# Optimization experiments

Measured on AMD Instinct MI355X. Metric: run time of the kernel, lower is better.

Reference implementation:

```python
import jax, jax.numpy as jnp
import numpy as np

B, N, IN_F, H, DEG, L = 4096, 64, 32, 128, 8, 2
E = N * DEG
ALPHA = 0.2  # LeakyReLU slope
EPS = 1e-5   # LayerNorm eps


def setup_inputs() -> dict:
    key = jax.random.key(0)
    ks = jax.random.split(key, 16)
    # ring graph: node i -> (i+k) mod N for k=1..DEG (unique edges, every node has out-edges)
    src = jnp.repeat(jnp.arange(N, dtype=jnp.int32), DEG)
    dst = ((src + jnp.tile(jnp.arange(1, DEG + 1, dtype=jnp.int32), N)) % N).astype(jnp.int32)
    edge_index = jnp.stack([src, dst])  # (2, E)
    Hh = H // 2
    inp = {
        "x": jax.random.normal(ks[0], (B, IN_F), jnp.float32),
        "station_idx": jax.random.randint(ks[1], (B,), 0, N, jnp.int32),
        "edge_index": edge_index,
        "edge_weight": jax.random.uniform(ks[2], (E,), jnp.float32, 0.1, 1.0),
        "Wp": jax.random.normal(ks[3], (IN_F, H), jnp.float32) / np.sqrt(IN_F),
        "bp": jnp.zeros((H,), jnp.float32),
        "emb": jax.random.normal(ks[4], (N, Hh), jnp.float32) * 0.02,
        "gat_W": jax.random.normal(ks[5], (L, H, H), jnp.float32) / np.sqrt(H),
        "gat_a": jax.random.normal(ks[6], (L, 2 * H), jnp.float32) * 0.1,
        "W1": jax.random.normal(ks[7], (H + Hh, H), jnp.float32) / np.sqrt(H + Hh),
        "b1": jnp.zeros((H,), jnp.float32),
        "g1": jnp.ones((H,), jnp.float32),
        "be1": jnp.zeros((H,), jnp.float32),
        "W2": jax.random.normal(ks[8], (H, Hh), jnp.float32) / np.sqrt(H),
        "b2": jnp.zeros((Hh,), jnp.float32),
        "g2": jnp.ones((Hh,), jnp.float32),
        "be2": jnp.zeros((Hh,), jnp.float32),
        "Wo": jax.random.normal(ks[9], (Hh, 1), jnp.float32) / np.sqrt(Hh),
        "bo": jnp.zeros((1,), jnp.float32),
    }
    return inp


def _layernorm(v, g, b):
    m = v.mean(-1, keepdims=True)
    var = ((v - m) ** 2).mean(-1, keepdims=True)
    return (v - m) / jnp.sqrt(var + EPS) * g + b


def _gat(h, W, a, src, dst, edge_weight):
    # h: (B, N, H); W: (H, H); a: (2H,)
    Wh = jnp.einsum('bnf,fg->bng', h, W)
    s_src = Wh @ a[:H]   # (B, N)
    s_dst = Wh @ a[H:]   # (B, N)
    e = jax.nn.leaky_relu(s_src[:, src] + s_dst[:, dst], ALPHA)  # (B, E)
    e = e * edge_weight[None, :]
    att = jnp.zeros((h.shape[0], N, N), h.dtype).at[:, src, dst].set(e)
    mask = att == 0  # faithfully reproduces the torch zero-mask trick
    att = jnp.where(mask, -jnp.inf, att)
    att = jax.nn.softmax(att, axis=2)
    att = jnp.where(mask, 0.0, att)
    # dropout is identity at inference
    return jax.nn.elu(jnp.einsum('bnm,bmf->bnf', att, Wh))


def reference(x, station_idx, edge_index, edge_weight, Wp, bp, emb, gat_W, gat_a,
              W1, b1, g1, be1, W2, b2, g2, be2, Wo, bo):
    src, dst = edge_index[0], edge_index[1]
    h0 = x @ Wp + bp                               # (B, H)
    h = jnp.broadcast_to(h0[:, None, :], (x.shape[0], N, H))
    for i in range(L):
        h = h + _gat(h, gat_W[i], gat_a[i], src, dst, edge_weight)
    h_node = h[jnp.arange(x.shape[0]), station_idx]  # (B, H)
    s = emb[station_idx]                              # (B, H//2)
    z = jnp.concatenate([h_node, s], axis=-1)
    z = jax.nn.relu(_layernorm(z @ W1 + b1, g1, be1))
    z = jax.nn.relu(_layernorm(z @ W2 + b2, g2, be2))
    return (z @ Wo + bo).squeeze(-1)                  # (B,)
```

## Files before the change

kernel.cpp:

```cpp
#include <hip/hip_runtime.h>
#include <math.h>

namespace {

constexpr int SPW  = 8;
constexpr int ACTW = 196;
constexpr float LNEPS = 1e-5f;

typedef __attribute__((ext_vector_type(8))) __bf16 bf16x8;
typedef __attribute__((ext_vector_type(4))) float  f32x4;

template<int V> struct ic { static constexpr int value = V; };

template<int N, int I = 0, class F>
__device__ __forceinline__ void sfor(F&& f) {
    if constexpr (I < N) { f(ic<I>{}); sfor<N, I + 1>(f); }
}

__device__ __forceinline__ float elu1(float v) {
    return v > 0.f ? v : (__expf(v) - 1.f);
}

__global__ __launch_bounds__(64) void pack_weights(
    const float* __restrict__ Wp, const float* __restrict__ gatW,
    const float* __restrict__ W1, const float* __restrict__ W2,
    __bf16* __restrict__ wsf)
{
    const int f = blockIdx.x;
    const int l = threadIdx.x;
    const float* src; int kt, nt, N;
    if (f < 8)        { src = Wp;            kt = 0;            nt = f;            N = 128; }
    else if (f < 40)  { int r = f - 8;  src = gatW;         kt = r >> 3; nt = r & 7; N = 128; }
    else if (f < 72)  { int r = f - 40; src = gatW + 16384; kt = r >> 3; nt = r & 7; N = 128; }
    else if (f < 120) { int r = f - 72; src = W1;           kt = r / 8;  nt = r % 8; N = 128; }
    else              { int r = f - 120; src = W2;          kt = r >> 2; nt = r & 3; N = 64;  }
    const int k0 = kt * 32 + (l >> 4) * 8;
    const int n  = nt * 16 + (l & 15);
    bf16x8 v;
    sfor<8>([&](auto E) {
        v[E.value] = (__bf16)src[(size_t)(k0 + E.value) * N + n];
    });
    *reinterpret_cast<bf16x8*>(wsf + ((size_t)f * 64 + l) * 8) = v;
}

__global__ __launch_bounds__(64) void mfma_fused(
    const float* __restrict__ x, const int* __restrict__ sid,
    const __bf16* __restrict__ wsf,
    const float* __restrict__ bp, const float* __restrict__ emb,
    const float* __restrict__ b1, const float* __restrict__ g1,
    const float* __restrict__ be1,
    const float* __restrict__ b2, const float* __restrict__ g2,
    const float* __restrict__ be2,
    const float* __restrict__ Wo, const float* __restrict__ bo,
    float* __restrict__ out)
{
    __shared__ float act[16 * ACTW];

    const int l  = threadIdx.x;
    const int gq = l >> 4;
    const int j  = l & 15;
    const int sbase = blockIdx.x * SPW;

    {
        const int s = l >> 2, ch = l & 3;
        float4 v0 = {0.f, 0.f, 0.f, 0.f}, v1 = v0;
        if (s < SPW) {
            const float* xp = x + (size_t)(sbase + s) * 32 + ch * 8;
            v0 = *reinterpret_cast<const float4*>(xp);
            v1 = *reinterpret_cast<const float4*>(xp + 4);
        }
        float* dst = act + s * ACTW + ch * 8;
        *reinterpret_cast<float4*>(dst)     = v0;
        *reinterpret_cast<float4*>(dst + 4) = v1;
    }

    auto gemm = [&]<int NKT, int NNT>(ic<NKT>, ic<NNT>, int fbase, f32x4 (&acc)[NNT]) {
        const __bf16* fb = wsf + ((size_t)fbase * 64 + l) * 8;
        bf16x8 bq0[NNT], bq1[NNT];
        auto ldkt = [&](auto KT, bf16x8 (&bq)[NNT]) {
            sfor<NNT>([&](auto NT) {
                bq[NT.value] = *reinterpret_cast<const bf16x8*>(
                    fb + (size_t)(decltype(KT)::value * NNT + NT.value) * 512);
            });
        };
        auto akt = [&](auto KT) -> bf16x8 {
            const float* p = act + j * ACTW + decltype(KT)::value * 32 + gq * 8;
            const float4 f0 = *reinterpret_cast<const float4*>(p);
            const float4 f1 = *reinterpret_cast<const float4*>(p + 4);
            bf16x8 a;
            a[0] = (__bf16)f0.x; a[1] = (__bf16)f0.y; a[2] = (__bf16)f0.z; a[3] = (__bf16)f0.w;
            a[4] = (__bf16)f1.x; a[5] = (__bf16)f1.y; a[6] = (__bf16)f1.z; a[7] = (__bf16)f1.w;
            return a;
        };
        auto mm = [&](bf16x8 a, bf16x8 (&bq)[NNT]) {
            sfor<NNT>([&](auto NT) {
                acc[NT.value] = __builtin_amdgcn_mfma_f32_16x16x32_bf16(
                    a, bq[NT.value], acc[NT.value], 0, 0, 0);
            });
        };
        ldkt(ic<0>{}, bq0);
        sfor<NKT>([&](auto KT) {
            constexpr int kt = decltype(KT)::value;
            if constexpr (kt + 1 < NKT) {
                if constexpr (((kt + 1) & 1) == 0) ldkt(ic<kt + 1>{}, bq0);
                else                               ldkt(ic<kt + 1>{}, bq1);
            }
            const bf16x8 a = akt(KT);
            if constexpr ((kt & 1) == 0) mm(a, bq0); else mm(a, bq1);
        });
    };

    auto writeC = [&](f32x4 (&C)[8]) {
        sfor<8>([&](auto NT) { sfor<4>([&](auto R) {
            act[(4 * gq + R.value) * ACTW + NT.value * 16 + j] = C[NT.value][R.value];
        }); });
    };

    float bpv[8];
    sfor<8>([&](auto NT) { bpv[NT.value] = bp[NT.value * 16 + j]; });

    f32x4 hC[8];

    {
        f32x4 acc[8] = {};
        gemm(ic<1>{}, ic<8>{}, 0, acc);
        sfor<8>([&](auto NT) { sfor<4>([&](auto R) {
            hC[NT.value][R.value] = acc[NT.value][R.value] + bpv[NT.value];
        }); });
    }
    writeC(hC);

    {
        f32x4 acc[8] = {};
        gemm(ic<4>{}, ic<8>{}, 8, acc);
        sfor<8>([&](auto NT) { sfor<4>([&](auto R) {
            hC[NT.value][R.value] += elu1(acc[NT.value][R.value]);
        }); });
    }
    writeC(hC);

    {
        f32x4 acc[8] = {};
        gemm(ic<4>{}, ic<8>{}, 40, acc);
        sfor<8>([&](auto NT) { sfor<4>([&](auto R) {
            hC[NT.value][R.value] += elu1(acc[NT.value][R.value]);
        }); });
    }
    writeC(hC);

    {
        const int s = l >> 2, ch = l & 3;
        float4 e0 = {0.f,0.f,0.f,0.f}, e1 = e0, e2 = e0, e3 = e0;
        if (s < SPW) {
            const int st = sid[sbase + s];
            const float* ep = emb + (size_t)st * 64 + ch * 16;
            e0 = *reinterpret_cast<const float4*>(ep);
            e1 = *reinterpret_cast<const float4*>(ep + 4);
            e2 = *reinterpret_cast<const float4*>(ep + 8);
            e3 = *reinterpret_cast<const float4*>(ep + 12);
        }
        float* dst = act + s * ACTW + 128 + ch * 16;
        *reinterpret_cast<float4*>(dst)      = e0;
        *reinterpret_cast<float4*>(dst + 4)  = e1;
        *reinterpret_cast<float4*>(dst + 8)  = e2;
        *reinterpret_cast<float4*>(dst + 12) = e3;
    }

    {
        f32x4 acc[8] = {};
        gemm(ic<6>{}, ic<8>{}, 72, acc);
        float b1v[8], g1v[8], be1v[8];
        sfor<8>([&](auto NT) {
            b1v[NT.value]  = b1[NT.value * 16 + j];
            g1v[NT.value]  = g1[NT.value * 16 + j];
            be1v[NT.value] = be1[NT.value * 16 + j];
        });
        float su[4] = {}, sq[4] = {};
        sfor<8>([&](auto NT) { sfor<4>([&](auto R) {
            const float u = acc[NT.value][R.value] + b1v[NT.value];
            acc[NT.value][R.value] = u;
            su[R.value] += u; sq[R.value] += u * u;
        }); });
#pragma unroll
        for (int off = 1; off <= 8; off <<= 1) {
            sfor<4>([&](auto R) {
                su[R.value] += __shfl_xor(su[R.value], off, 64);
                sq[R.value] += __shfl_xor(sq[R.value], off, 64);
            });
        }
        float m[4], rs[4];
        sfor<4>([&](auto R) {
            m[R.value] = su[R.value] * (1.f / 128.f);
            const float var = sq[R.value] * (1.f / 128.f) - m[R.value] * m[R.value];
            rs[R.value] = rsqrtf(var + LNEPS);
        });
        sfor<8>([&](auto NT) { sfor<4>([&](auto R) {
            const float z = fmaxf((acc[NT.value][R.value] - m[R.value]) * rs[R.value]
                                  * g1v[NT.value] + be1v[NT.value], 0.f);
            act[(4 * gq + R.value) * ACTW + NT.value * 16 + j] = z;
        }); });
    }

    {
        f32x4 acc[4] = {};
        gemm(ic<4>{}, ic<4>{}, 120, acc);
        float b2v[4], g2v[4], be2v[4], wov[4];
        sfor<4>([&](auto NT) {
            b2v[NT.value]  = b2[NT.value * 16 + j];
            g2v[NT.value]  = g2[NT.value * 16 + j];
            be2v[NT.value] = be2[NT.value * 16 + j];
            wov[NT.value]  = Wo[NT.value * 16 + j];
        });
        float su[4] = {}, sq[4] = {};
        sfor<4>([&](auto NT) { sfor<4>([&](auto R) {
            const float v = acc[NT.value][R.value] + b2v[NT.value];
            acc[NT.value][R.value] = v;
            su[R.value] += v; sq[R.value] += v * v;
        }); });
#pragma unroll
        for (int off = 1; off <= 8; off <<= 1) {
            sfor<4>([&](auto R) {
                su[R.value] += __shfl_xor(su[R.value], off, 64);
                sq[R.value] += __shfl_xor(sq[R.value], off, 64);
            });
        }
        float po[4];
        sfor<4>([&](auto R) {
            const float m   = su[R.value] * (1.f / 64.f);
            const float var = sq[R.value] * (1.f / 64.f) - m * m;
            const float rs  = rsqrtf(var + LNEPS);
            float p = 0.f;
            sfor<4>([&](auto NT) {
                p += fmaxf((acc[NT.value][R.value] - m) * rs * g2v[NT.value]
                           + be2v[NT.value], 0.f) * wov[NT.value];
            });
            po[R.value] = p;
        });
#pragma unroll
        for (int off = 1; off <= 8; off <<= 1) {
            sfor<4>([&](auto R) { po[R.value] += __shfl_xor(po[R.value], off, 64); });
        }
        const float bov = bo[0];
        if (j == 0 && gq < 2) {
            sfor<4>([&](auto R) {
                out[sbase + 4 * gq + R.value] = po[R.value] + bov;
            });
        }
    }
}

}

extern "C" void kernel_launch(void* const* d_in, const int* in_sizes, int n_in,
                              void* d_out, int out_size, void* d_ws, size_t ws_size,
                              hipStream_t stream)
{
    const float* x    = (const float*)d_in[0];
    const int*   sid  = (const int*)d_in[1];
    const float* Wp   = (const float*)d_in[4];
    const float* bp   = (const float*)d_in[5];
    const float* emb  = (const float*)d_in[6];
    const float* gatW = (const float*)d_in[7];
    const float* W1   = (const float*)d_in[9];
    const float* b1   = (const float*)d_in[10];
    const float* g1   = (const float*)d_in[11];
    const float* be1  = (const float*)d_in[12];
    const float* W2   = (const float*)d_in[13];
    const float* b2   = (const float*)d_in[14];
    const float* g2   = (const float*)d_in[15];
    const float* be2  = (const float*)d_in[16];
    const float* Wo   = (const float*)d_in[17];
    const float* bo   = (const float*)d_in[18];
    float* out = (float*)d_out;

    __bf16* wsf = (__bf16*)d_ws;

    pack_weights<<<dim3(136), dim3(64), 0, stream>>>(Wp, gatW, W1, W2, wsf);
    mfma_fused<<<dim3(4096 / SPW), dim3(64), 0, stream>>>(
        x, sid, wsf, bp, emb, b1, g1, be1, b2, g2, be2, Wo, bo, out);
}
```

Measured before the change: 101.7 us.

## Stage packed GAT/MLP weights in LDS shared by two waves per block

Each block now runs two waves over 16 samples and cooperatively copies the packed bf16 GAT, W1 and W2 weight fragments (128KB) into LDS once. Later GEMMs read their B fragments from LDS instead of global/L2. The projection weights are preloaded into registers, and the x, station id and embedding loads are hoisted to the kernel start. The cost is a serialized prologue copy and roughly 150KB of LDS per block, which allows only one block per CU and halves the number of blocks.

```diff
diff --git a/kernel.cpp b/kernel.cpp
--- a/kernel.cpp
+++ b/kernel.cpp
@@ -43,7 +43,7 @@
     *reinterpret_cast<bf16x8*>(wsf + ((size_t)f * 64 + l) * 8) = v;
 }
 
-__global__ __launch_bounds__(64) void mfma_fused(
+__global__ __launch_bounds__(128) void mfma_fused(
     const float* __restrict__ x, const int* __restrict__ sid,
     const __bf16* __restrict__ wsf,
     const float* __restrict__ bp, const float* __restrict__ emb,
@@ -54,43 +54,80 @@
     const float* __restrict__ Wo, const float* __restrict__ bo,
     float* __restrict__ out)
 {
-    __shared__ float act[16 * ACTW];
-
-    const int l  = threadIdx.x;
-    const int gq = l >> 4;
-    const int j  = l & 15;
-    const int sbase = blockIdx.x * SPW;
-
-    {
-        const int s = l >> 2, ch = l & 3;
-        float4 v0 = {0.f, 0.f, 0.f, 0.f}, v1 = v0;
+    __shared__ __align__(16) __bf16 wlds[128 * 512];
+    __shared__ __align__(16) float  actbuf[2][16 * ACTW];
+
+    const int tid = threadIdx.x;
+    const int l   = tid & 63;
+    const int w   = tid >> 6;
+    const int gq  = l >> 4;
+    const int j   = l & 15;
+    const int sbase = (blockIdx.x * 2 + w) * SPW;
+    float* A = actbuf[w];
+
+    const int s  = l >> 2, ch = l & 3;
+    float4 xv0 = {0,0,0,0}, xv1 = xv0;
+    int st = 0;
+    if (s < SPW) {
+        const float* xp = x + (size_t)(sbase + s) * 32 + ch * 8;
+        xv0 = *reinterpret_cast<const float4*>(xp);
+        xv1 = *reinterpret_cast<const float4*>(xp + 4);
+        st  = sid[sbase + s];
+    }
+    bf16x8 wpf[8];
+    sfor<8>([&](auto NT) {
+        wpf[NT.value] = *reinterpret_cast<const bf16x8*>(
+            wsf + ((size_t)NT.value * 64 + l) * 8);
+    });
+    float bpv[8];
+    sfor<8>([&](auto NT) { bpv[NT.value] = bp[NT.value * 16 + j]; });
+
+    {
+        const float4* gW = reinterpret_cast<const float4*>(wsf)
+                         + (size_t)(8 + w * 64) * 64 + l;
+        float4* sW = reinterpret_cast<float4*>(wlds) + (size_t)(w * 64) * 64 + l;
+#pragma unroll 8
+        for (int i = 0; i < 64; ++i) sW[(size_t)i * 64] = gW[(size_t)i * 64];
+    }
+
+    {
+        float* dst = A + s * ACTW + ch * 8;
+        *reinterpret_cast<float4*>(dst)     = xv0;
+        *reinterpret_cast<float4*>(dst + 4) = xv1;
+        float4 e0 = {0,0,0,0}, e1 = e0, e2 = e0, e3 = e0;
         if (s < SPW) {
-            const float* xp = x + (size_t)(sbase + s) * 32 + ch * 8;
-            v0 = *reinterpret_cast<const float4*>(xp);
-            v1 = *reinterpret_cast<const float4*>(xp + 4);
-        }
-        float* dst = act + s * ACTW + ch * 8;
-        *reinterpret_cast<float4*>(dst)     = v0;
-        *reinterpret_cast<float4*>(dst + 4) = v1;
-    }
+            const float* ep = emb + (size_t)st * 64 + ch * 16;
+            e0 = *reinterpret_cast<const float4*>(ep);
+            e1 = *reinterpret_cast<const float4*>(ep + 4);
+            e2 = *reinterpret_cast<const float4*>(ep + 8);
+            e3 = *reinterpret_cast<const float4*>(ep + 12);
+        }
+        float* ed = A + s * ACTW + 128 + ch * 16;
+        *reinterpret_cast<float4*>(ed)      = e0;
+        *reinterpret_cast<float4*>(ed + 4)  = e1;
+        *reinterpret_cast<float4*>(ed + 8)  = e2;
+        *reinterpret_cast<float4*>(ed + 12) = e3;
+    }
+    __syncthreads();
+
+    auto akt = [&]<int KT>(ic<KT>) -> bf16x8 {
+        const float* p = A + j * ACTW + KT * 32 + gq * 8;
+        const float4 f0 = *reinterpret_cast<const float4*>(p);
+        const float4 f1 = *reinterpret_cast<const float4*>(p + 4);
+        bf16x8 a;
+        a[0] = (__bf16)f0.x; a[1] = (__bf16)f0.y; a[2] = (__bf16)f0.z; a[3] = (__bf16)f0.w;
+        a[4] = (__bf16)f1.x; a[5] = (__bf16)f1.y; a[6] = (__bf16)f1.z; a[7] = (__bf16)f1.w;
+        return a;
+    };
 
     auto gemm = [&]<int NKT, int NNT>(ic<NKT>, ic<NNT>, int fbase, f32x4 (&acc)[NNT]) {
-        const __bf16* fb = wsf + ((size_t)fbase * 64 + l) * 8;
+        const __bf16* fb = wlds + (size_t)fbase * 512 + (size_t)l * 8;
         bf16x8 bq0[NNT], bq1[NNT];
         auto ldkt = [&](auto KT, bf16x8 (&bq)[NNT]) {
             sfor<NNT>([&](auto NT) {
                 bq[NT.value] = *reinterpret_cast<const bf16x8*>(
                     fb + (size_t)(decltype(KT)::value * NNT + NT.value) * 512);
             });
-        };
-        auto akt = [&](auto KT) -> bf16x8 {
-            const float* p = act + j * ACTW + decltype(KT)::value * 32 + gq * 8;
-            const float4 f0 = *reinterpret_cast<const float4*>(p);
-            const float4 f1 = *reinterpret_cast<const float4*>(p + 4);
-            bf16x8 a;
-            a[0] = (__bf16)f0.x; a[1] = (__bf16)f0.y; a[2] = (__bf16)f0.z; a[3] = (__bf16)f0.w;
-            a[4] = (__bf16)f1.x; a[5] = (__bf16)f1.y; a[6] = (__bf16)f1.z; a[7] = (__bf16)f1.w;
-            return a;
         };
         auto mm = [&](bf16x8 a, bf16x8 (&bq)[NNT]) {
             sfor<NNT>([&](auto NT) {
@@ -105,25 +142,26 @@
                 if constexpr (((kt + 1) & 1) == 0) ldkt(ic<kt + 1>{}, bq0);
                 else                               ldkt(ic<kt + 1>{}, bq1);
             }
-            const bf16x8 a = akt(KT);
+            const bf16x8 a = akt(ic<kt>{});
             if constexpr ((kt & 1) == 0) mm(a, bq0); else mm(a, bq1);
         });
     };
 
     auto writeC = [&](f32x4 (&C)[8]) {
         sfor<8>([&](auto NT) { sfor<4>([&](auto R) {
-            act[(4 * gq + R.value) * ACTW + NT.value * 16 + j] = C[NT.value][R.value];
+            A[(4 * gq + R.value) * ACTW + NT.value * 16 + j] = C[NT.value][R.value];
         }); });
     };
 
-    float bpv[8];
-    sfor<8>([&](auto NT) { bpv[NT.value] = bp[NT.value * 16 + j]; });
-
     f32x4 hC[8];
 
     {
         f32x4 acc[8] = {};
-        gemm(ic<1>{}, ic<8>{}, 0, acc);
+        const bf16x8 a = akt(ic<0>{});
+        sfor<8>([&](auto NT) {
+            acc[NT.value] = __builtin_amdgcn_mfma_f32_16x16x32_bf16(
+                a, wpf[NT.value], acc[NT.value], 0, 0, 0);
+        });
         sfor<8>([&](auto NT) { sfor<4>([&](auto R) {
             hC[NT.value][R.value] = acc[NT.value][R.value] + bpv[NT.value];
         }); });
@@ -132,7 +170,7 @@
 
     {
         f32x4 acc[8] = {};
-        gemm(ic<4>{}, ic<8>{}, 8, acc);
+        gemm(ic<4>{}, ic<8>{}, 0, acc);
         sfor<8>([&](auto NT) { sfor<4>([&](auto R) {
             hC[NT.value][R.value] += elu1(acc[NT.value][R.value]);
         }); });
@@ -141,7 +179,7 @@
 
     {
         f32x4 acc[8] = {};
-        gemm(ic<4>{}, ic<8>{}, 40, acc);
+        gemm(ic<4>{}, ic<8>{}, 32, acc);
         sfor<8>([&](auto NT) { sfor<4>([&](auto R) {
             hC[NT.value][R.value] += elu1(acc[NT.value][R.value]);
         }); });
@@ -149,26 +187,8 @@
     writeC(hC);
 
     {
-        const int s = l >> 2, ch = l & 3;
-        float4 e0 = {0.f,0.f,0.f,0.f}, e1 = e0, e2 = e0, e3 = e0;
-        if (s < SPW) {
-            const int st = sid[sbase + s];
-            const float* ep = emb + (size_t)st * 64 + ch * 16;
-            e0 = *reinterpret_cast<const float4*>(ep);
-            e1 = *reinterpret_cast<const float4*>(ep + 4);
-            e2 = *reinterpret_cast<const float4*>(ep + 8);
-            e3 = *reinterpret_cast<const float4*>(ep + 12);
-        }
-        float* dst = act + s * ACTW + 128 + ch * 16;
-        *reinterpret_cast<float4*>(dst)      = e0;
-        *reinterpret_cast<float4*>(dst + 4)  = e1;
-        *reinterpret_cast<float4*>(dst + 8)  = e2;
-        *reinterpret_cast<float4*>(dst + 12) = e3;
-    }
-
-    {
         f32x4 acc[8] = {};
-        gemm(ic<6>{}, ic<8>{}, 72, acc);
+        gemm(ic<6>{}, ic<8>{}, 64, acc);
         float b1v[8], g1v[8], be1v[8];
         sfor<8>([&](auto NT) {
             b1v[NT.value]  = b1[NT.value * 16 + j];
@@ -197,13 +217,13 @@
         sfor<8>([&](auto NT) { sfor<4>([&](auto R) {
             const float z = fmaxf((acc[NT.value][R.value] - m[R.value]) * rs[R.value]
                                   * g1v[NT.value] + be1v[NT.value], 0.f);
-            act[(4 * gq + R.value) * ACTW + NT.value * 16 + j] = z;
+            A[(4 * gq + R.value) * ACTW + NT.value * 16 + j] = z;
         }); });
     }
 
     {
         f32x4 acc[4] = {};
-        gemm(ic<4>{}, ic<4>{}, 120, acc);
+        gemm(ic<4>{}, ic<4>{}, 112, acc);
         float b2v[4], g2v[4], be2v[4], wov[4];
         sfor<4>([&](auto NT) {
             b2v[NT.value]  = b2[NT.value * 16 + j];
@@ -276,6 +296,6 @@
     __bf16* wsf = (__bf16*)d_ws;
 
     pack_weights<<<dim3(136), dim3(64), 0, stream>>>(Wp, gatW, W1, W2, wsf);
-    mfma_fused<<<dim3(4096 / SPW), dim3(64), 0, stream>>>(
+    mfma_fused<<<dim3(4096 / (2 * SPW)), dim3(128), 0, stream>>>(
         x, sid, wsf, bp, emb, b1, g1, be1, b2, g2, be2, Wo, bo, out);
 }
```

Result: no change. 102.4 us (+0.7%).
